# Performance work log

Hardware: AMD Instinct MI355X
Metric: run time of the kernel (lower is better)

Reference implementation:

```python
import jax, jax.numpy as jnp
import numpy as np
from jax import lax

KH, KW, K = 3, 3, 9
PAD, BN_EPS = 1, 1e-5


def setup_inputs() -> dict:
    key = jax.random.key(0)
    ks = jax.random.split(key, 10)
    B, CHI, CHO, H, W = 2, 64, 64, 128, 128
    x = jax.random.normal(ks[0], (B, CHI, H, W), dtype=jnp.float32)
    # offset/mask branch conv: 3*K output channels (o1, o2, mask)
    w_off = jax.random.normal(ks[1], (3 * K, CHI, KH, KW), dtype=jnp.float32) * 0.01
    b_off = jax.random.normal(ks[2], (3 * K,), dtype=jnp.float32) * 0.01
    # main deformable conv weight/bias
    fan = CHI * K
    weight = jax.random.normal(ks[3], (CHO, CHI, KH, KW), dtype=jnp.float32) / np.sqrt(fan)
    bias = jax.random.normal(ks[4], (CHO,), dtype=jnp.float32) * 0.01
    # BatchNorm (eval-mode) params
    gamma = jax.random.uniform(ks[5], (CHO,), minval=0.5, maxval=1.5, dtype=jnp.float32)
    beta = jax.random.normal(ks[6], (CHO,), dtype=jnp.float32) * 0.1
    run_mean = jax.random.normal(ks[7], (CHO,), dtype=jnp.float32) * 0.1
    run_var = jax.random.uniform(ks[8], (CHO,), minval=0.5, maxval=1.5, dtype=jnp.float32)
    return {"x": x, "w_off": w_off, "b_off": b_off, "weight": weight,
            "bias": bias, "gamma": gamma, "beta": beta,
            "run_mean": run_mean, "run_var": run_var}


def _dcn_bn_relu(x, w_off, b_off, weight, bias, gamma, beta, run_mean, run_var):
    B, C, H, W = x.shape
    CHO = weight.shape[0]
    # offset/mask branch: regular 3x3 conv, stride 1, pad 1
    om = lax.conv_general_dilated(
        x, w_off, window_strides=(1, 1), padding=[(PAD, PAD), (PAD, PAD)],
        dimension_numbers=("NCHW", "OIHW", "NCHW")) + b_off[None, :, None, None]
    o1, o2, m = jnp.split(om, 3, axis=1)          # each [B, K, H, W]
    offset = jnp.concatenate([o1, o2], axis=1)    # [B, 2K, H, W]
    off_y = offset[:, 0::2]                       # interleaved (y, x) per tap, as in DCNv2 CUDA
    off_x = offset[:, 1::2]
    mask = jax.nn.sigmoid(m)                      # [B, K, H, W] modulation

    # sampling positions: p = p0 + p_k + offset
    ky, kx = jnp.meshgrid(jnp.arange(KH), jnp.arange(KW), indexing="ij")
    ky = ky.reshape(K).astype(x.dtype)
    kx = kx.reshape(K).astype(x.dtype)
    hh = jnp.arange(H, dtype=x.dtype)
    ww = jnp.arange(W, dtype=x.dtype)
    py = hh[None, None, :, None] - PAD + ky[None, :, None, None] + off_y  # [B,K,H,W]
    px = ww[None, None, None, :] - PAD + kx[None, :, None, None] + off_x

    y0f = jnp.floor(py)
    x0f = jnp.floor(px)
    ly = (py - y0f)[..., None]
    lx = (px - x0f)[..., None]
    y0 = y0f.astype(jnp.int32)
    x0 = x0f.astype(jnp.int32)
    bidx = jnp.arange(B)[:, None, None, None]

    def gather(yi, xi):
        valid = ((yi >= 0) & (yi < H) & (xi >= 0) & (xi < W)).astype(x.dtype)
        yc = jnp.clip(yi, 0, H - 1)
        xc = jnp.clip(xi, 0, W - 1)
        g = x[bidx, :, yc, xc]                    # [B, K, H, W, C]
        return g * valid[..., None]

    v00 = gather(y0, x0)
    v01 = gather(y0, x0 + 1)
    v10 = gather(y0 + 1, x0)
    v11 = gather(y0 + 1, x0 + 1)
    sampled = (v00 * (1 - ly) * (1 - lx) + v01 * (1 - ly) * lx
               + v10 * ly * (1 - lx) + v11 * ly * lx)
    sampled = sampled * mask[..., None]           # modulated

    out = jnp.einsum("bkhwc,ock->bohw", sampled,
                     weight.reshape(CHO, C, K)) + bias[None, :, None, None]

    # eval-mode BatchNorm + ReLU
    inv = gamma / jnp.sqrt(run_var + BN_EPS)
    out = (out - run_mean[None, :, None, None]) * inv[None, :, None, None] \
          + beta[None, :, None, None]
    return jax.nn.relu(out)


def reference(x, w_off, b_off, weight, bias, gamma, beta, run_mean, run_var):
    return _dcn_bn_relu(x, w_off, b_off, weight, bias, gamma, beta, run_mean, run_var)
```

## Files before the change

kernel.cpp:

```cpp
#include <hip/hip_runtime.h>
#include <hip/hip_bf16.h>

#define HH 128
#define WW 128
#define CI 64
#define CO 64
#define SLS 584
#define HPS 72
#define HALW 18

typedef __attribute__((ext_vector_type(8))) short short8;
typedef __attribute__((ext_vector_type(4))) float floatx4;

__device__ __forceinline__ unsigned short f2bf(float f) {
  union { float f; unsigned u; } uu; uu.f = f;
  unsigned r = uu.u + 0x7FFFu + ((uu.u >> 16) & 1u);
  return (unsigned short)(r >> 16);
}
__device__ __forceinline__ unsigned pack2bf(float lo, float hi) {
  return (unsigned)f2bf(lo) | ((unsigned)f2bf(hi) << 16);
}
__device__ __forceinline__ float bfl(unsigned u) { return __uint_as_float(u << 16); }
__device__ __forceinline__ float bfh(unsigned u) { return __uint_as_float(u & 0xffff0000u); }

__global__ __launch_bounds__(256) void prep_kernel(
    const float* __restrict__ x, unsigned* __restrict__ xTb_u,
    const float* __restrict__ weight, const float* __restrict__ bias,
    const float* __restrict__ gamma, const float* __restrict__ beta,
    const float* __restrict__ mean, const float* __restrict__ var,
    const float* __restrict__ w_off, const float* __restrict__ b_off,
    unsigned short* __restrict__ Wm, unsigned short* __restrict__ w2,
    float* __restrict__ bias2, float* __restrict__ boff2) {
  __shared__ unsigned T2[32 * 33];
  int bid = blockIdx.x;
  int tid = threadIdx.x;
  if (bid < 1024) {
    int b = bid >> 9, h = (bid >> 2) & 127, q = bid & 3;
    int cp = tid >> 3, wc = tid & 7;
    const float* xp = x + (((long)(b * CI + 2 * cp) * HH + h) * WW + q * 32 + wc * 4);
    float4 a0 = *(const float4*)xp;
    float4 a1 = *(const float4*)(xp + HH * WW);
    T2[(wc * 4 + 0) * 33 + cp] = pack2bf(a0.x, a1.x);
    T2[(wc * 4 + 1) * 33 + cp] = pack2bf(a0.y, a1.y);
    T2[(wc * 4 + 2) * 33 + cp] = pack2bf(a0.z, a1.z);
    T2[(wc * 4 + 3) * 33 + cp] = pack2bf(a0.w, a1.w);
    __syncthreads();
    int px = tid >> 3, g = tid & 7;
    const unsigned* src = &T2[px * 33 + g * 4];
    unsigned* dst = xTb_u + ((long)((b * HH + h) * WW + q * 32 + px)) * 32 + g * 4;
    *(uint4*)dst = make_uint4(src[0], src[1], src[2], src[3]);
    return;
  }
  int idx = (bid - 1024) * 256 + tid;
  if (idx < 32) boff2[idx] = (idx < 27) ? b_off[idx] : 0.f;
  if (idx >= CO * 576) return;
  int o = idx / 576, kc = idx - o * 576;
  int k = kc >> 6, c = kc & 63;
  float inv = gamma[o] * rsqrtf(var[o] + 1e-5f);
  Wm[idx] = f2bf(weight[(o * CI + c) * 9 + k] * inv);
  if (kc == 0) bias2[o] = (bias[o] - mean[o]) * inv + beta[o];
  if (o < 27) w2[idx] = f2bf(w_off[o * 576 + c * 9 + k]);
  else if (o < 32) w2[idx] = 0;
}

__global__ __launch_bounds__(256, 8) void dcn_kernel(
    const unsigned short* __restrict__ xTb,
    const unsigned short* __restrict__ w2, const float* __restrict__ boff2,
    const unsigned short* __restrict__ Wm, const float* __restrict__ bias2,
    float* __restrict__ out) {
  __shared__ char smem[18688];
  short* hal = (short*)smem;
  __hip_bfloat16* SL = (__hip_bfloat16*)smem;
  float* omL = (float*)(smem + 14016);

  int bid = blockIdx.x;
  int s = bid & 7;
  int n = bid >> 3;
  int b = n >> 7;
  int rem = n & 127;
  int h = s * 16 + (rem >> 3);
  int w0 = (rem & 7) * 16;
  int tid = threadIdx.x, lane = tid & 63, wave = tid >> 6;

#pragma unroll
  for (int it = 0; it < 2; it++) {
    int t = it * 256 + tid;
    if (t < 432) {
      int row = t / 144;
      int r2 = t - row * 144;
      int xi = r2 >> 3, cg = r2 & 7;
      int y = h - 1 + row, xx = w0 - 1 + xi;
      uint4 v = make_uint4(0u, 0u, 0u, 0u);
      if ((unsigned)y < (unsigned)HH && (unsigned)xx < (unsigned)WW)
        v = *(const uint4*)(xTb + (long)((b * HH + y) * WW + xx) * CI + cg * 8);
      *(uint4*)(hal + (row * HALW + xi) * HPS + cg * 8) = v;
    }
  }
  __syncthreads();

  {
    int r16 = lane & 15, quad = lane >> 4;
    int m16 = wave & 1, kh = wave >> 1;
    floatx4 t0 = {0.f, 0.f, 0.f, 0.f};
    floatx4 t1 = {0.f, 0.f, 0.f, 0.f};
    if (kh == 0) t0 = *(const floatx4*)(boff2 + m16 * 16 + quad * 4);
    const short* ap = (const short*)(w2 + (m16 * 16 + r16) * 576 + kh * 32 + quad * 8);
#pragma unroll
    for (int kk = 0; kk < 9; kk++) {
      int dy = kk / 3, dxk = kk - 3 * dy;
      short8 bfrag = *(const short8*)(hal + (dy * HALW + r16 + dxk) * HPS + kh * 32 + quad * 8);
      short8 afrag = *(const short8*)(ap + kk * 64);
      if (kk & 1)
        t1 = __builtin_amdgcn_mfma_f32_16x16x32_bf16(afrag, bfrag, t1, 0, 0, 0);
      else
        t0 = __builtin_amdgcn_mfma_f32_16x16x32_bf16(afrag, bfrag, t0, 0, 0, 0);
    }
    floatx4 t = t0 + t1;
    *(floatx4*)(omL + kh * 576 + r16 * 36 + m16 * 16 + quad * 4) = t;
  }
  __syncthreads();

  float pwx = 0.f, pwy = 0.f, pwz = 0.f, pww = 0.f;
  int pov = 0;
  if (lane < 36) {
    int p_loc = (lane * 7282) >> 16;
    int k = lane - p_loc * 9;
    int p = wave * 4 + p_loc;
    const float* o0 = omL + p * 36;
    const float* o1 = omL + 576 + p * 36;
    float oy = o0[2 * k] + o1[2 * k];
    float ox = o0[2 * k + 1] + o1[2 * k + 1];
    float mm = o0[18 + k] + o1[18 + k];
    float msk = 1.f / (1.f + __expf(-mm));
    int ky = (k * 11) >> 5;
    int kx = k - 3 * ky;
    float py = (float)(h - 1 + ky) + oy;
    float pxx = (float)(w0 + p - 1 + kx) + ox;
    float y0f = floorf(py), x0f = floorf(pxx);
    float ly = py - y0f, lx = pxx - x0f;
    int y0 = (int)y0f, x0 = (int)x0f;
    int y1 = y0 + 1, x1 = x0 + 1;
    float lylx = ly * lx;
    bool y0v = (unsigned)y0 < (unsigned)HH, y1v = (unsigned)y1 < (unsigned)HH;
    bool x0v = (unsigned)x0 < (unsigned)WW, x1v = (unsigned)x1 < (unsigned)WW;
    int yc0 = min(max(y0, 0), HH - 1), yc1 = min(max(y1, 0), HH - 1);
    int xc0 = min(max(x0, 0), WW - 1), xc1 = min(max(x1, 0), WW - 1);
    pwx = (y0v && x0v) ? (1.f - ly - lx + lylx) * msk : 0.f;
    pwy = (y0v && x1v) ? (lx - lylx) * msk : 0.f;
    pwz = (y1v && x0v) ? (ly - lylx) * msk : 0.f;
    pww = (y1v && x1v) ? lylx * msk : 0.f;
    int off00 = (yc0 * WW + xc0) * CI;
    int dxs = (xc1 - xc0) * CI;
    int dys = (yc1 - yc0) * WW * CI;
    pov = off00 | ((dxs >> 6) << 20) | ((dys >> 13) << 21);
  }
  __syncthreads();

  {
    int cq = lane & 15, pl = lane >> 4;
    int p = wave * 4 + pl;
    const unsigned short* xb = xTb + (long)b * (HH * WW * CI);
    uint2 uA[3][4], uB[2][4], uC[2][4], uD[2][4];

#define LOADK(U, kk)                                  \
    {                                                 \
      int v = __shfl(pov, pl * 9 + (kk));             \
      int o00 = (v & 0xFFFFF) + cq * 4;               \
      int dxv = (v >> 14) & 64;                       \
      int dyv = (v >> 8) & 8192;                      \
      U[0] = *(const uint2*)(xb + o00);               \
      U[1] = *(const uint2*)(xb + o00 + dxv);         \
      U[2] = *(const uint2*)(xb + o00 + dyv);         \
      U[3] = *(const uint2*)(xb + o00 + dyv + dxv);   \
    }

#define COMBK(U, kk)                                                                          \
    {                                                                                         \
      int src = pl * 9 + (kk);                                                                \
      float wx = __shfl(pwx, src), wy = __shfl(pwy, src);                                     \
      float wz = __shfl(pwz, src), ww = __shfl(pww, src);                                     \
      float lo0 = bfl(U[0].x) * wx + bfl(U[1].x) * wy + bfl(U[2].x) * wz + bfl(U[3].x) * ww;  \
      float hi0 = bfh(U[0].x) * wx + bfh(U[1].x) * wy + bfh(U[2].x) * wz + bfh(U[3].x) * ww;  \
      float lo1 = bfl(U[0].y) * wx + bfl(U[1].y) * wy + bfl(U[2].y) * wz + bfl(U[3].y) * ww;  \
      float hi1 = bfh(U[0].y) * wx + bfh(U[1].y) * wy + bfh(U[2].y) * wz + bfh(U[3].y) * ww;  \
      unsigned r0, r1;                                                                        \
      asm("v_cvt_pk_bf16_f32 %0, %1, %2" : "=v"(r0) : "v"(lo0), "v"(hi0));                    \
      asm("v_cvt_pk_bf16_f32 %0, %1, %2" : "=v"(r1) : "v"(lo1), "v"(hi1));                    \
      *(uint2*)(&SL[p * SLS + (kk) * 64 + cq * 4]) = make_uint2(r0, r1);                      \
    }

    LOADK(uA[0], 0) LOADK(uA[1], 1) LOADK(uA[2], 2)
    LOADK(uB[0], 3) LOADK(uB[1], 4)
    COMBK(uA[0], 0) COMBK(uA[1], 1) COMBK(uA[2], 2)
    LOADK(uC[0], 5) LOADK(uC[1], 6)
    COMBK(uB[0], 3) COMBK(uB[1], 4)
    LOADK(uD[0], 7) LOADK(uD[1], 8)
    COMBK(uC[0], 5) COMBK(uC[1], 6)
    COMBK(uD[0], 7) COMBK(uD[1], 8)
#undef LOADK
#undef COMBK
  }
  __syncthreads();

  {
    int r16 = lane & 15, quad = lane >> 4;
    floatx4 acc0 = *(const floatx4*)(bias2 + wave * 16 + quad * 4);
    floatx4 acc1 = {0.f, 0.f, 0.f, 0.f};
    const unsigned short* Ap = Wm + (wave * 16 + r16) * 576 + quad * 8;
    const __hip_bfloat16* Sp = &SL[r16 * SLS + quad * 8];
#pragma unroll
    for (int kc0 = 0; kc0 < 576; kc0 += 64) {
      short8 av0 = *(const short8*)(Ap + kc0);
      short8 bv0 = *(const short8*)(Sp + kc0);
      acc0 = __builtin_amdgcn_mfma_f32_16x16x32_bf16(av0, bv0, acc0, 0, 0, 0);
      short8 av1 = *(const short8*)(Ap + kc0 + 32);
      short8 bv1 = *(const short8*)(Sp + kc0 + 32);
      acc1 = __builtin_amdgcn_mfma_f32_16x16x32_bf16(av1, bv1, acc1, 0, 0, 0);
    }
    floatx4 acc = acc0 + acc1;
#pragma unroll
    for (int r = 0; r < 4; r++) {
      int o = wave * 16 + quad * 4 + r;
      out[((b * CO + o) * HH + h) * WW + w0 + r16] = fmaxf(acc[r], 0.f);
    }
  }
}

extern "C" void kernel_launch(void* const* d_in, const int* in_sizes, int n_in,
                              void* d_out, int out_size, void* d_ws, size_t ws_size,
                              hipStream_t stream) {
  const float* x = (const float*)d_in[0];
  const float* w_off = (const float*)d_in[1];
  const float* b_off = (const float*)d_in[2];
  const float* weight = (const float*)d_in[3];
  const float* bias = (const float*)d_in[4];
  const float* gamma = (const float*)d_in[5];
  const float* beta = (const float*)d_in[6];
  const float* run_mean = (const float*)d_in[7];
  const float* run_var = (const float*)d_in[8];
  float* outp = (float*)d_out;

  char* ws = (char*)d_ws;
  unsigned* xTb = (unsigned*)ws;
  unsigned short* Wm = (unsigned short*)(ws + 4194304);
  unsigned short* w2 = (unsigned short*)(ws + 4268032);
  float* bias2 = (float*)(ws + 4304896);
  float* boff2 = (float*)(ws + 4305152);

  prep_kernel<<<1168, 256, 0, stream>>>(x, xTb, weight, bias, gamma, beta,
                                        run_mean, run_var, w_off, b_off,
                                        Wm, w2, bias2, boff2);
  dcn_kernel<<<2048, 256, 0, stream>>>((const unsigned short*)xTb, w2, boff2,
                                       Wm, bias2, outp);
}
```

Baseline: 111.7 us.

## Split fused DCN kernel into offset kernel and sampling/GEMM kernel

Splits the single fused kernel into two. One kernel computes the offset/mask convolution and writes per-tap bilinear weights and packed gather offsets to global workspace. A second kernel reloads them into shared memory and does the sampling and the main GEMM. The aim is lower shared-memory and register pressure in each kernel, allowing higher occupancy, at the cost of an extra launch and a global round trip of about 6.5 MB of intermediate data.

```diff
diff --git a/kernel.cpp b/kernel.cpp
--- a/kernel.cpp
+++ b/kernel.cpp
@@ -63,15 +63,12 @@
   else if (o < 32) w2[idx] = 0;
 }
 
-__global__ __launch_bounds__(256, 8) void dcn_kernel(
+__global__ __launch_bounds__(256) void off_kernel(
     const unsigned short* __restrict__ xTb,
     const unsigned short* __restrict__ w2, const float* __restrict__ boff2,
-    const unsigned short* __restrict__ Wm, const float* __restrict__ bias2,
-    float* __restrict__ out) {
-  __shared__ char smem[18688];
-  short* hal = (short*)smem;
-  __hip_bfloat16* SL = (__hip_bfloat16*)smem;
-  float* omL = (float*)(smem + 14016);
+    float4* __restrict__ Pw4, int* __restrict__ PoI) {
+  __shared__ short hal[3 * HALW * HPS];
+  __shared__ float omL[2 * 16 * 36];
 
   int bid = blockIdx.x;
   int s = bid & 7;
@@ -120,8 +117,6 @@
   }
   __syncthreads();
 
-  float pwx = 0.f, pwy = 0.f, pwz = 0.f, pww = 0.f;
-  int pov = 0;
   if (lane < 36) {
     int p_loc = (lane * 7282) >> 16;
     int k = lane - p_loc * 9;
@@ -145,27 +140,54 @@
     bool x0v = (unsigned)x0 < (unsigned)WW, x1v = (unsigned)x1 < (unsigned)WW;
     int yc0 = min(max(y0, 0), HH - 1), yc1 = min(max(y1, 0), HH - 1);
     int xc0 = min(max(x0, 0), WW - 1), xc1 = min(max(x1, 0), WW - 1);
-    pwx = (y0v && x0v) ? (1.f - ly - lx + lylx) * msk : 0.f;
-    pwy = (y0v && x1v) ? (lx - lylx) * msk : 0.f;
-    pwz = (y1v && x0v) ? (ly - lylx) * msk : 0.f;
-    pww = (y1v && x1v) ? lylx * msk : 0.f;
+    float wx = (y0v && x0v) ? (1.f - ly - lx + lylx) * msk : 0.f;
+    float wy = (y0v && x1v) ? (lx - lylx) * msk : 0.f;
+    float wz = (y1v && x0v) ? (ly - lylx) * msk : 0.f;
+    float ww = (y1v && x1v) ? lylx * msk : 0.f;
     int off00 = (yc0 * WW + xc0) * CI;
     int dxs = (xc1 - xc0) * CI;
     int dys = (yc1 - yc0) * WW * CI;
-    pov = off00 | ((dxs >> 6) << 20) | ((dys >> 13) << 21);
+    int gi = (((b * HH + h) * WW + w0) + p) * 9 + k;
+    Pw4[gi] = make_float4(wx, wy, wz, ww);
+    PoI[gi] = off00 | ((dxs >> 6) << 20) | ((dys >> 13) << 21);
+  }
+}
+
+__global__ __launch_bounds__(256) void gemm_kernel(
+    const unsigned short* __restrict__ xTb, const float4* __restrict__ Pw4,
+    const int* __restrict__ PoI, const unsigned short* __restrict__ Wm,
+    const float* __restrict__ bias2, float* __restrict__ out) {
+  __shared__ __hip_bfloat16 SL[16 * SLS];
+  __shared__ float4 PwL[144];
+  __shared__ int PoL[144];
+
+  int bid = blockIdx.x;
+  int s = bid & 7;
+  int n = bid >> 3;
+  int b = n >> 7;
+  int rem = n & 127;
+  int h = s * 16 + (rem >> 3);
+  int w0 = (rem & 7) * 16;
+  int tid = threadIdx.x, lane = tid & 63, wave = tid >> 6;
+  int rowpix = (b * HH + h) * WW + w0;
+
+  if (tid < 144) {
+    PwL[tid] = Pw4[rowpix * 9 + tid];
+    PoL[tid] = PoI[rowpix * 9 + tid];
   }
   __syncthreads();
 
   {
     int cq = lane & 15, pl = lane >> 4;
     int p = wave * 4 + pl;
+    int ch = cq * 4;
     const unsigned short* xb = xTb + (long)b * (HH * WW * CI);
     uint2 uA[3][4], uB[2][4], uC[2][4], uD[2][4];
 
 #define LOADK(U, kk)                                  \
     {                                                 \
-      int v = __shfl(pov, pl * 9 + (kk));             \
-      int o00 = (v & 0xFFFFF) + cq * 4;               \
+      int v = PoL[p * 9 + (kk)];                      \
+      int o00 = (v & 0xFFFFF) + ch;                   \
       int dxv = (v >> 14) & 64;                       \
       int dyv = (v >> 8) & 8192;                      \
       U[0] = *(const uint2*)(xb + o00);               \
@@ -176,9 +198,8 @@
 
 #define COMBK(U, kk)                                                                          \
     {                                                                                         \
-      int src = pl * 9 + (kk);                                                                \
-      float wx = __shfl(pwx, src), wy = __shfl(pwy, src);                                     \
-      float wz = __shfl(pwz, src), ww = __shfl(pww, src);                                     \
+      float4 wv = PwL[p * 9 + (kk)];                                                          \
+      float wx = wv.x, wy = wv.y, wz = wv.z, ww = wv.w;                                       \
       float lo0 = bfl(U[0].x) * wx + bfl(U[1].x) * wy + bfl(U[2].x) * wz + bfl(U[3].x) * ww;  \
       float hi0 = bfh(U[0].x) * wx + bfh(U[1].x) * wy + bfh(U[2].x) * wz + bfh(U[3].x) * ww;  \
       float lo1 = bfl(U[0].y) * wx + bfl(U[1].y) * wy + bfl(U[2].y) * wz + bfl(U[3].y) * ww;  \
@@ -186,7 +207,7 @@
       unsigned r0, r1;                                                                        \
       asm("v_cvt_pk_bf16_f32 %0, %1, %2" : "=v"(r0) : "v"(lo0), "v"(hi0));                    \
       asm("v_cvt_pk_bf16_f32 %0, %1, %2" : "=v"(r1) : "v"(lo1), "v"(hi1));                    \
-      *(uint2*)(&SL[p * SLS + (kk) * 64 + cq * 4]) = make_uint2(r0, r1);                      \
+      *(uint2*)(&SL[p * SLS + (kk) * 64 + ch]) = make_uint2(r0, r1);                          \
     }
 
     LOADK(uA[0], 0) LOADK(uA[1], 1) LOADK(uA[2], 2)
@@ -246,10 +267,14 @@
   unsigned short* w2 = (unsigned short*)(ws + 4268032);
   float* bias2 = (float*)(ws + 4304896);
   float* boff2 = (float*)(ws + 4305152);
+  float4* Pw4 = (float4*)(ws + 4305280);
+  int* PoI = (int*)(ws + 9023872);
 
   prep_kernel<<<1168, 256, 0, stream>>>(x, xTb, weight, bias, gamma, beta,
                                         run_mean, run_var, w_off, b_off,
                                         Wm, w2, bias2, boff2);
-  dcn_kernel<<<2048, 256, 0, stream>>>((const unsigned short*)xTb, w2, boff2,
-                                       Wm, bias2, outp);
-}
+  off_kernel<<<2048, 256, 0, stream>>>((const unsigned short*)xTb, w2, boff2,
+                                       Pw4, PoI);
+  gemm_kernel<<<2048, 256, 0, stream>>>((const unsigned short*)xTb, Pw4, PoI,
+                                        Wm, bias2, outp);
+}
```

Measured after the change: 117.5 us. +5.2%, slower.

## Process two 16-pixel tiles per block to halve grid size

Applied to the files above, without the earlier changes.

Each block now handles two adjacent 16-pixel tiles (32 pixels) of a row, using doubled shared memory and looping over both tiles in every phase. The grid is halved and launch bounds lowered to 4 blocks per SM. This amortises per-block overhead, barriers and weight fragment loads across twice the work, and gives more independent memory loads per block. The cost is higher LDS and register use per block and therefore lower occupancy.

```diff
diff --git a/kernel.cpp b/kernel.cpp
--- a/kernel.cpp
+++ b/kernel.cpp
@@ -8,6 +8,7 @@
 #define SLS 584
 #define HPS 72
 #define HALW 18
+#define TS 18688
 
 typedef __attribute__((ext_vector_type(8))) short short8;
 typedef __attribute__((ext_vector_type(4))) float floatx4;
@@ -63,36 +64,36 @@
   else if (o < 32) w2[idx] = 0;
 }
 
-__global__ __launch_bounds__(256, 8) void dcn_kernel(
+__global__ __launch_bounds__(256, 4) void dcn_kernel(
     const unsigned short* __restrict__ xTb,
     const unsigned short* __restrict__ w2, const float* __restrict__ boff2,
     const unsigned short* __restrict__ Wm, const float* __restrict__ bias2,
     float* __restrict__ out) {
-  __shared__ char smem[18688];
-  short* hal = (short*)smem;
-  __hip_bfloat16* SL = (__hip_bfloat16*)smem;
-  float* omL = (float*)(smem + 14016);
+  __shared__ char smem[2 * TS];
 
   int bid = blockIdx.x;
   int s = bid & 7;
   int n = bid >> 3;
-  int b = n >> 7;
-  int rem = n & 127;
-  int h = s * 16 + (rem >> 3);
-  int w0 = (rem & 7) * 16;
+  int b = n >> 6;
+  int rem = n & 63;
+  int h = s * 16 + (rem >> 2);
+  int w00 = (rem & 3) * 32;
   int tid = threadIdx.x, lane = tid & 63, wave = tid >> 6;
 
 #pragma unroll
-  for (int it = 0; it < 2; it++) {
+  for (int it = 0; it < 4; it++) {
     int t = it * 256 + tid;
-    if (t < 432) {
-      int row = t / 144;
-      int r2 = t - row * 144;
+    if (t < 864) {
+      int ti = (t >= 432);
+      int tt = t - ti * 432;
+      int row = tt / 144;
+      int r2 = tt - row * 144;
       int xi = r2 >> 3, cg = r2 & 7;
-      int y = h - 1 + row, xx = w0 - 1 + xi;
+      int y = h - 1 + row, xx = w00 + ti * 16 - 1 + xi;
       uint4 v = make_uint4(0u, 0u, 0u, 0u);
       if ((unsigned)y < (unsigned)HH && (unsigned)xx < (unsigned)WW)
         v = *(const uint4*)(xTb + (long)((b * HH + y) * WW + xx) * CI + cg * 8);
+      short* hal = (short*)(smem + ti * TS);
       *(uint4*)(hal + (row * HALW + xi) * HPS + cg * 8) = v;
     }
   }
@@ -101,71 +102,82 @@
   {
     int r16 = lane & 15, quad = lane >> 4;
     int m16 = wave & 1, kh = wave >> 1;
-    floatx4 t0 = {0.f, 0.f, 0.f, 0.f};
-    floatx4 t1 = {0.f, 0.f, 0.f, 0.f};
-    if (kh == 0) t0 = *(const floatx4*)(boff2 + m16 * 16 + quad * 4);
-    const short* ap = (const short*)(w2 + (m16 * 16 + r16) * 576 + kh * 32 + quad * 8);
-#pragma unroll
-    for (int kk = 0; kk < 9; kk++) {
-      int dy = kk / 3, dxk = kk - 3 * dy;
-      short8 bfrag = *(const short8*)(hal + (dy * HALW + r16 + dxk) * HPS + kh * 32 + quad * 8);
-      short8 afrag = *(const short8*)(ap + kk * 64);
-      if (kk & 1)
-        t1 = __builtin_amdgcn_mfma_f32_16x16x32_bf16(afrag, bfrag, t1, 0, 0, 0);
-      else
-        t0 = __builtin_amdgcn_mfma_f32_16x16x32_bf16(afrag, bfrag, t0, 0, 0, 0);
-    }
-    floatx4 t = t0 + t1;
-    *(floatx4*)(omL + kh * 576 + r16 * 36 + m16 * 16 + quad * 4) = t;
-  }
-  __syncthreads();
-
-  float pwx = 0.f, pwy = 0.f, pwz = 0.f, pww = 0.f;
-  int pov = 0;
+#pragma unroll
+    for (int ti = 0; ti < 2; ti++) {
+      short* hal = (short*)(smem + ti * TS);
+      float* omL = (float*)(smem + ti * TS + 14016);
+      floatx4 t0 = {0.f, 0.f, 0.f, 0.f};
+      floatx4 t1 = {0.f, 0.f, 0.f, 0.f};
+      if (kh == 0) t0 = *(const floatx4*)(boff2 + m16 * 16 + quad * 4);
+      const short* ap = (const short*)(w2 + (m16 * 16 + r16) * 576 + kh * 32 + quad * 8);
+#pragma unroll
+      for (int kk = 0; kk < 9; kk++) {
+        int dy = kk / 3, dxk = kk - 3 * dy;
+        short8 bfrag = *(const short8*)(hal + (dy * HALW + r16 + dxk) * HPS + kh * 32 + quad * 8);
+        short8 afrag = *(const short8*)(ap + kk * 64);
+        if (kk & 1)
+          t1 = __builtin_amdgcn_mfma_f32_16x16x32_bf16(afrag, bfrag, t1, 0, 0, 0);
+        else
+          t0 = __builtin_amdgcn_mfma_f32_16x16x32_bf16(afrag, bfrag, t0, 0, 0, 0);
+      }
+      floatx4 t = t0 + t1;
+      *(floatx4*)(omL + kh * 576 + r16 * 36 + m16 * 16 + quad * 4) = t;
+    }
+  }
+  __syncthreads();
+
+  float pwx[2] = {0.f, 0.f}, pwy[2] = {0.f, 0.f}, pwz[2] = {0.f, 0.f}, pww[2] = {0.f, 0.f};
+  int pov[2] = {0, 0};
   if (lane < 36) {
     int p_loc = (lane * 7282) >> 16;
     int k = lane - p_loc * 9;
     int p = wave * 4 + p_loc;
-    const float* o0 = omL + p * 36;
-    const float* o1 = omL + 576 + p * 36;
-    float oy = o0[2 * k] + o1[2 * k];
-    float ox = o0[2 * k + 1] + o1[2 * k + 1];
-    float mm = o0[18 + k] + o1[18 + k];
-    float msk = 1.f / (1.f + __expf(-mm));
     int ky = (k * 11) >> 5;
     int kx = k - 3 * ky;
-    float py = (float)(h - 1 + ky) + oy;
-    float pxx = (float)(w0 + p - 1 + kx) + ox;
-    float y0f = floorf(py), x0f = floorf(pxx);
-    float ly = py - y0f, lx = pxx - x0f;
-    int y0 = (int)y0f, x0 = (int)x0f;
-    int y1 = y0 + 1, x1 = x0 + 1;
-    float lylx = ly * lx;
-    bool y0v = (unsigned)y0 < (unsigned)HH, y1v = (unsigned)y1 < (unsigned)HH;
-    bool x0v = (unsigned)x0 < (unsigned)WW, x1v = (unsigned)x1 < (unsigned)WW;
-    int yc0 = min(max(y0, 0), HH - 1), yc1 = min(max(y1, 0), HH - 1);
-    int xc0 = min(max(x0, 0), WW - 1), xc1 = min(max(x1, 0), WW - 1);
-    pwx = (y0v && x0v) ? (1.f - ly - lx + lylx) * msk : 0.f;
-    pwy = (y0v && x1v) ? (lx - lylx) * msk : 0.f;
-    pwz = (y1v && x0v) ? (ly - lylx) * msk : 0.f;
-    pww = (y1v && x1v) ? lylx * msk : 0.f;
-    int off00 = (yc0 * WW + xc0) * CI;
-    int dxs = (xc1 - xc0) * CI;
-    int dys = (yc1 - yc0) * WW * CI;
-    pov = off00 | ((dxs >> 6) << 20) | ((dys >> 13) << 21);
+#pragma unroll
+    for (int ti = 0; ti < 2; ti++) {
+      const float* omL = (const float*)(smem + ti * TS + 14016);
+      int w0 = w00 + ti * 16;
+      const float* o0 = omL + p * 36;
+      const float* o1 = omL + 576 + p * 36;
+      float oy = o0[2 * k] + o1[2 * k];
+      float ox = o0[2 * k + 1] + o1[2 * k + 1];
+      float mm = o0[18 + k] + o1[18 + k];
+      float msk = 1.f / (1.f + __expf(-mm));
+      float py = (float)(h - 1 + ky) + oy;
+      float pxx = (float)(w0 + p - 1 + kx) + ox;
+      float y0f = floorf(py), x0f = floorf(pxx);
+      float ly = py - y0f, lx = pxx - x0f;
+      int y0 = (int)y0f, x0 = (int)x0f;
+      int y1 = y0 + 1, x1 = x0 + 1;
+      float lylx = ly * lx;
+      bool y0v = (unsigned)y0 < (unsigned)HH, y1v = (unsigned)y1 < (unsigned)HH;
+      bool x0v = (unsigned)x0 < (unsigned)WW, x1v = (unsigned)x1 < (unsigned)WW;
+      int yc0 = min(max(y0, 0), HH - 1), yc1 = min(max(y1, 0), HH - 1);
+      int xc0 = min(max(x0, 0), WW - 1), xc1 = min(max(x1, 0), WW - 1);
+      pwx[ti] = (y0v && x0v) ? (1.f - ly - lx + lylx) * msk : 0.f;
+      pwy[ti] = (y0v && x1v) ? (lx - lylx) * msk : 0.f;
+      pwz[ti] = (y1v && x0v) ? (ly - lylx) * msk : 0.f;
+      pww[ti] = (y1v && x1v) ? lylx * msk : 0.f;
+      int off00 = (yc0 * WW + xc0) * CI;
+      int dxs = (xc1 - xc0) * CI;
+      int dys = (yc1 - yc0) * WW * CI;
+      pov[ti] = off00 | ((dxs >> 6) << 20) | ((dys >> 13) << 21);
+    }
   }
   __syncthreads();
 
   {
     int cq = lane & 15, pl = lane >> 4;
     int p = wave * 4 + pl;
+    int ch = cq * 4;
     const unsigned short* xb = xTb + (long)b * (HH * WW * CI);
     uint2 uA[3][4], uB[2][4], uC[2][4], uD[2][4];
 
 #define LOADK(U, kk)                                  \
     {                                                 \
-      int v = __shfl(pov, pl * 9 + (kk));             \
-      int o00 = (v & 0xFFFFF) + cq * 4;               \
+      int v = __shfl(povt, pl * 9 + (kk));            \
+      int o00 = (v & 0xFFFFF) + ch;                   \
       int dxv = (v >> 14) & 64;                       \
       int dyv = (v >> 8) & 8192;                      \
       U[0] = *(const uint2*)(xb + o00);               \
@@ -177,8 +189,8 @@
 #define COMBK(U, kk)                                                                          \
     {                                                                                         \
       int src = pl * 9 + (kk);                                                                \
-      float wx = __shfl(pwx, src), wy = __shfl(pwy, src);                                     \
-      float wz = __shfl(pwz, src), ww = __shfl(pww, src);                                     \
+      float wx = __shfl(pwxt, src), wy = __shfl(pwyt, src);                                   \
+      float wz = __shfl(pwzt, src), ww = __shfl(pwwt, src);                                   \
       float lo0 = bfl(U[0].x) * wx + bfl(U[1].x) * wy + bfl(U[2].x) * wz + bfl(U[3].x) * ww;  \
       float hi0 = bfh(U[0].x) * wx + bfh(U[1].x) * wy + bfh(U[2].x) * wz + bfh(U[3].x) * ww;  \
       float lo1 = bfl(U[0].y) * wx + bfl(U[1].y) * wy + bfl(U[2].y) * wz + bfl(U[3].y) * ww;  \
@@ -186,17 +198,23 @@
       unsigned r0, r1;                                                                        \
       asm("v_cvt_pk_bf16_f32 %0, %1, %2" : "=v"(r0) : "v"(lo0), "v"(hi0));                    \
       asm("v_cvt_pk_bf16_f32 %0, %1, %2" : "=v"(r1) : "v"(lo1), "v"(hi1));                    \
-      *(uint2*)(&SL[p * SLS + (kk) * 64 + cq * 4]) = make_uint2(r0, r1);                      \
-    }
-
-    LOADK(uA[0], 0) LOADK(uA[1], 1) LOADK(uA[2], 2)
-    LOADK(uB[0], 3) LOADK(uB[1], 4)
-    COMBK(uA[0], 0) COMBK(uA[1], 1) COMBK(uA[2], 2)
-    LOADK(uC[0], 5) LOADK(uC[1], 6)
-    COMBK(uB[0], 3) COMBK(uB[1], 4)
-    LOADK(uD[0], 7) LOADK(uD[1], 8)
-    COMBK(uC[0], 5) COMBK(uC[1], 6)
-    COMBK(uD[0], 7) COMBK(uD[1], 8)
+      *(uint2*)(&SL[p * SLS + (kk) * 64 + ch]) = make_uint2(r0, r1);                          \
+    }
+
+#pragma unroll
+    for (int ti = 0; ti < 2; ti++) {
+      __hip_bfloat16* SL = (__hip_bfloat16*)(smem + ti * TS);
+      int povt = pov[ti];
+      float pwxt = pwx[ti], pwyt = pwy[ti], pwzt = pwz[ti], pwwt = pww[ti];
+      LOADK(uA[0], 0) LOADK(uA[1], 1) LOADK(uA[2], 2)
+      LOADK(uB[0], 3) LOADK(uB[1], 4)
+      COMBK(uA[0], 0) COMBK(uA[1], 1) COMBK(uA[2], 2)
+      LOADK(uC[0], 5) LOADK(uC[1], 6)
+      COMBK(uB[0], 3) COMBK(uB[1], 4)
+      LOADK(uD[0], 7) LOADK(uD[1], 8)
+      COMBK(uC[0], 5) COMBK(uC[1], 6)
+      COMBK(uD[0], 7) COMBK(uD[1], 8)
+    }
 #undef LOADK
 #undef COMBK
   }
@@ -204,24 +222,29 @@
 
   {
     int r16 = lane & 15, quad = lane >> 4;
-    floatx4 acc0 = *(const floatx4*)(bias2 + wave * 16 + quad * 4);
-    floatx4 acc1 = {0.f, 0.f, 0.f, 0.f};
+    floatx4 binit = *(const floatx4*)(bias2 + wave * 16 + quad * 4);
     const unsigned short* Ap = Wm + (wave * 16 + r16) * 576 + quad * 8;
-    const __hip_bfloat16* Sp = &SL[r16 * SLS + quad * 8];
-#pragma unroll
-    for (int kc0 = 0; kc0 < 576; kc0 += 64) {
-      short8 av0 = *(const short8*)(Ap + kc0);
-      short8 bv0 = *(const short8*)(Sp + kc0);
-      acc0 = __builtin_amdgcn_mfma_f32_16x16x32_bf16(av0, bv0, acc0, 0, 0, 0);
-      short8 av1 = *(const short8*)(Ap + kc0 + 32);
-      short8 bv1 = *(const short8*)(Sp + kc0 + 32);
-      acc1 = __builtin_amdgcn_mfma_f32_16x16x32_bf16(av1, bv1, acc1, 0, 0, 0);
-    }
-    floatx4 acc = acc0 + acc1;
-#pragma unroll
-    for (int r = 0; r < 4; r++) {
-      int o = wave * 16 + quad * 4 + r;
-      out[((b * CO + o) * HH + h) * WW + w0 + r16] = fmaxf(acc[r], 0.f);
+#pragma unroll
+    for (int ti = 0; ti < 2; ti++) {
+      const __hip_bfloat16* SL = (const __hip_bfloat16*)(smem + ti * TS);
+      const __hip_bfloat16* Sp = &SL[r16 * SLS + quad * 8];
+      floatx4 acc0 = binit;
+      floatx4 acc1 = {0.f, 0.f, 0.f, 0.f};
+#pragma unroll
+      for (int kc0 = 0; kc0 < 576; kc0 += 64) {
+        short8 av0 = *(const short8*)(Ap + kc0);
+        short8 bv0 = *(const short8*)(Sp + kc0);
+        acc0 = __builtin_amdgcn_mfma_f32_16x16x32_bf16(av0, bv0, acc0, 0, 0, 0);
+        short8 av1 = *(const short8*)(Ap + kc0 + 32);
+        short8 bv1 = *(const short8*)(Sp + kc0 + 32);
+        acc1 = __builtin_amdgcn_mfma_f32_16x16x32_bf16(av1, bv1, acc1, 0, 0, 0);
+      }
+      floatx4 acc = acc0 + acc1;
+#pragma unroll
+      for (int r = 0; r < 4; r++) {
+        int o = wave * 16 + quad * 4 + r;
+        out[((b * CO + o) * HH + h) * WW + w00 + ti * 16 + r16] = fmaxf(acc[r], 0.f);
+      }
     }
   }
 }
@@ -250,6 +273,6 @@
   prep_kernel<<<1168, 256, 0, stream>>>(x, xTb, weight, bias, gamma, beta,
                                         run_mean, run_var, w_off, b_off,
                                         Wm, w2, bias2, boff2);
-  dcn_kernel<<<2048, 256, 0, stream>>>((const unsigned short*)xTb, w2, boff2,
+  dcn_kernel<<<1024, 256, 0, stream>>>((const unsigned short*)xTb, w2, boff2,
                                        Wm, bias2, outp);
 }
```

New measurement: 110.6 us. Within noise of the previous version (-0.9%).
